# Kernel optimization log

Hardware: AMD Instinct MI355X
Metric: run time of the kernel (lower is better)

The kernel has to match this reference:

```python
import jax, jax.numpy as jnp
import numpy as np

N = 2_000_000
F = 32  # feature_num
GH = GW = 256


def _bilinear_interpolate(grid, coords):
    # grid: [H, W, F], coords: [N, 2] in (0,1)
    W = grid.shape[1] - 1
    H = grid.shape[0] - 1
    x = coords[:, 0] * W
    y = coords[:, 1] * H
    x0 = x.astype(jnp.int32)
    y0 = y.astype(jnp.int32)
    xf = x % 1
    yf = y % 1
    x1 = jnp.minimum(x0 + 1, W)
    y1 = jnp.minimum(y0 + 1, H)
    tl = grid[y0, x0]  # [N, F]
    tr = grid[y0, x1]
    bl = grid[y1, x0]
    br = grid[y1, x1]
    top = (1 - xf)[:, None] * tl + xf[:, None] * tr
    bot = (1 - xf)[:, None] * bl + xf[:, None] * br
    return (1 - yf)[:, None] * top + yf[:, None] * bot


def setup_inputs() -> dict:
    key = jax.random.key(0)
    ks = jax.random.split(key, 16)
    inp = {
        "pos": jax.random.uniform(ks[0], (N, 2), dtype=jnp.float32),
        "dir": jax.random.uniform(ks[1], (N, 2), dtype=jnp.float32),
        # grids: randn * 10 as in the torch module
        "pos_grid": jax.random.normal(ks[2], (GH, GW, F), dtype=jnp.float32) * 10.0,
        "dir_grid": jax.random.normal(ks[3], (GH, GW, F), dtype=jnp.float32) * 10.0,
        # shared encoder: Linear(2,4), Linear(4,3)
        "enc_w1": jax.random.normal(ks[4], (2, 4), dtype=jnp.float32) * 0.5,
        "enc_b1": jax.random.normal(ks[5], (4,), dtype=jnp.float32) * 0.1,
        "enc_w2": jax.random.normal(ks[6], (4, 3), dtype=jnp.float32) * 0.5,
        "enc_b2": jax.random.normal(ks[7], (3,), dtype=jnp.float32) * 0.1,
        # fc head: 2F -> 64 -> 16 -> 8 -> 3
        "fc_w1": jax.random.normal(ks[8], (2 * F, 64), dtype=jnp.float32) * 0.1,
        "fc_b1": jnp.zeros((64,), dtype=jnp.float32),
        "fc_w2": jax.random.normal(ks[9], (64, 16), dtype=jnp.float32) * 0.1,
        "fc_b2": jnp.zeros((16,), dtype=jnp.float32),
        "fc_w3": jax.random.normal(ks[10], (16, 8), dtype=jnp.float32) * 0.1,
        "fc_b3": jnp.zeros((8,), dtype=jnp.float32),
        "fc_w4": jax.random.normal(ks[11], (8, 3), dtype=jnp.float32) * 0.1,
        "fc_b4": jnp.zeros((3,), dtype=jnp.float32),
    }
    return inp


def reference(pos, dir, pos_grid, dir_grid,
              enc_w1, enc_b1, enc_w2, enc_b2,
              fc_w1, fc_b1, fc_w2, fc_b2, fc_w3, fc_b3, fc_w4, fc_b4):
    def encoder(x):
        h = jnp.tanh(x @ enc_w1 + enc_b1)
        return jax.nn.sigmoid(h @ enc_w2 + enc_b2)  # [N, 3]; only cols 0,1 used

    p = encoder(pos)
    d = encoder(dir)
    # features are .detach()'ed in the original
    pos_feat = jax.lax.stop_gradient(_bilinear_interpolate(pos_grid, p))
    dir_feat = jax.lax.stop_gradient(_bilinear_interpolate(dir_grid, d))
    x = jnp.concatenate([pos_feat, dir_feat], axis=1)  # [N, 2F]
    # Dropout layers are identity in eval mode
    x = jax.nn.leaky_relu(x @ fc_w1 + fc_b1)
    x = jax.nn.leaky_relu(x @ fc_w2 + fc_b2)
    x = jax.nn.leaky_relu(x @ fc_w3 + fc_b3)
    x = jax.nn.leaky_relu(x @ fc_w4 + fc_b4)
    return jax.nn.sigmoid(x) * 255.0
```

## Files before the change

kernel.cpp:

```cpp
#include <hip/hip_runtime.h>
#include <math.h>

typedef __attribute__((ext_vector_type(8))) __bf16 bf16x8;
typedef __attribute__((ext_vector_type(4))) __bf16 bf16x4;
typedef __attribute__((ext_vector_type(4))) short short4v;
typedef __attribute__((ext_vector_type(4))) float floatx4;
typedef __attribute__((ext_vector_type(8))) float floatx8;

__device__ __forceinline__ float fast_rcp(float x) { return __builtin_amdgcn_rcpf(x); }
__device__ __forceinline__ float sigmoidf_(float z) { return fast_rcp(1.0f + __expf(-z)); }
__device__ __forceinline__ float fast_tanh(float z) {
    float e = __expf(2.0f * z);
    return 1.0f - 2.0f * fast_rcp(e + 1.0f);
}
__device__ __forceinline__ float leaky(float v) { return fmaxf(v, 0.01f * v); }

__device__ __forceinline__ int swzb(int row, int byteoff) {
    return row * 128 + (byteoff ^ ((row & 7) << 4));
}

__global__ void convert_grids(const float* __restrict__ g0, const float* __restrict__ g1,
                              __bf16* __restrict__ o0, __bf16* __restrict__ o1, int elems) {
    int i = blockIdx.x * blockDim.x + threadIdx.x;
    int nvec = elems >> 2;
    if (i < nvec) {
        float4 v = ((const float4*)g0)[i];
        bf16x4 r = { (__bf16)v.x, (__bf16)v.y, (__bf16)v.z, (__bf16)v.w };
        ((bf16x4*)o0)[i] = r;
    } else if (i < 2 * nvec) {
        int j = i - nvec;
        float4 v = ((const float4*)g1)[j];
        bf16x4 r = { (__bf16)v.x, (__bf16)v.y, (__bf16)v.z, (__bf16)v.w };
        ((bf16x4*)o1)[j] = r;
    }
}

template<bool BF16G>
__global__ __launch_bounds__(256, 3) void gridnet_fwd(
    const float2* __restrict__ pos, const float2* __restrict__ dir_,
    const float* __restrict__ pos_gridf, const float* __restrict__ dir_gridf,
    const __bf16* __restrict__ pos_gridb, const __bf16* __restrict__ dir_gridb,
    const float* __restrict__ enc_w1, const float* __restrict__ enc_b1,
    const float* __restrict__ enc_w2, const float* __restrict__ enc_b2,
    const float* __restrict__ fc_w1, const float* __restrict__ fc_b1,
    const float* __restrict__ fc_w2, const float* __restrict__ fc_b2,
    const float* __restrict__ fc_w3, const float* __restrict__ fc_b3,
    const float* __restrict__ fc_w4, const float* __restrict__ fc_b4,
    float* __restrict__ out, int n)
{
    __shared__ __align__(1024) char smem[8192 + 2048 + 4 * 5120];
    __shared__ float b1lds[64];
    __shared__ float b2lds[16];

    const int tid  = threadIdx.x;
    const int lane = tid & 63;
    const int wid  = tid >> 6;
    const int quad = lane >> 4;
    const int l15  = lane & 15;

    char* W1p = smem;
    char* W2p = smem + 8192;
    float* H2f = (float*)(smem + 10240 + wid * 5120);

    for (int idx = tid; idx < 4096; idx += 256)
        *(__bf16*)(W1p + swzb(idx & 63, (idx >> 6) * 2)) = (__bf16)fc_w1[idx];
    for (int idx = tid; idx < 1024; idx += 256)
        *(__bf16*)(W2p + swzb(idx & 15, (idx >> 4) * 2)) = (__bf16)fc_w2[idx];
    if (tid < 64) b1lds[tid] = fc_b1[tid];
    if (tid < 16) b2lds[tid] = fc_b2[tid];
    __syncthreads();

    bf16x8 wf[2][4];
    #pragma unroll
    for (int ks = 0; ks < 2; ++ks)
        #pragma unroll
        for (int mt = 0; mt < 4; ++mt)
            wf[ks][mt] = *(const bf16x8*)(W1p + swzb(mt * 16 + l15, ks * 64 + quad * 16));
    short4v w2a[4];
    #pragma unroll
    for (int kb = 0; kb < 4; ++kb)
        w2a[kb] = *(const short4v*)(W2p + swzb(l15, kb * 32 + quad * 8));
    floatx4 b1v[4];
    #pragma unroll
    for (int mt = 0; mt < 4; ++mt)
        b1v[mt] = *(const floatx4*)(b1lds + mt * 16 + quad * 4);
    floatx4 b2v = *(const floatx4*)(b2lds + quad * 4);

    int i  = blockIdx.x * 256 + wid * 64 + lane;
    int ic = min(i, n - 1);

    unsigned pcp[2];
    float xfp[2], yfp[2];
    #pragma unroll
    for (int pass = 0; pass < 2; ++pass) {
        float2 xy = pass ? dir_[ic] : pos[ic];
        float hh[4];
        #pragma unroll
        for (int k = 0; k < 4; ++k)
            hh[k] = fast_tanh(xy.x * enc_w1[k] + xy.y * enc_w1[4 + k] + enc_b1[k]);
        float e0 = enc_b2[0], e1 = enc_b2[1];
        #pragma unroll
        for (int k = 0; k < 4; ++k) {
            e0 += hh[k] * enc_w2[3 * k + 0];
            e1 += hh[k] * enc_w2[3 * k + 1];
        }
        float x = sigmoidf_(e0) * 255.0f;
        float y = sigmoidf_(e1) * 255.0f;
        int x0 = (int)x, y0 = (int)y;
        xfp[pass] = x - (float)x0;
        yfp[pass] = y - (float)y0;
        int x1 = min(x0 + 1, 255), y1 = min(y0 + 1, 255);
        pcp[pass] = (unsigned)x0 | ((unsigned)y0 << 8) | ((unsigned)x1 << 16) | ((unsigned)y1 << 24);
    }

    bf16x8 xfr[2][4];
    #pragma unroll
    for (int ks = 0; ks < 2; ++ks) {
        #pragma unroll
        for (int nt = 0; nt < 4; ++nt) {
            const int src = nt * 16 + l15;
            unsigned pcq = (unsigned)__shfl((int)pcp[ks], src);
            float xfq = __shfl(xfp[ks], src);
            float yfq = __shfl(yfp[ks], src);
            int x0 = pcq & 255, y0 = (pcq >> 8) & 255;
            int x1 = (pcq >> 16) & 255, y1 = pcq >> 24;
            float oxf = 1.0f - xfq, oyf = 1.0f - yfq;
            floatx8 r;
            if (BF16G) {
                const __bf16* ga = (ks ? dir_gridb : pos_gridb) + quad * 8;
                bf16x8 va = *(const bf16x8*)(ga + (((y0 << 8) + x0) << 5));
                bf16x8 vb = *(const bf16x8*)(ga + (((y0 << 8) + x1) << 5));
                bf16x8 vc = *(const bf16x8*)(ga + (((y1 << 8) + x0) << 5));
                bf16x8 vd = *(const bf16x8*)(ga + (((y1 << 8) + x1) << 5));
                r = (oyf * oxf) * __builtin_convertvector(va, floatx8)
                  + (oyf * xfq) * __builtin_convertvector(vb, floatx8)
                  + (yfq * oxf) * __builtin_convertvector(vc, floatx8)
                  + (yfq * xfq) * __builtin_convertvector(vd, floatx8);
            } else {
                const float* ga = (ks ? dir_gridf : pos_gridf) + quad * 8;
                floatx8 va = *(const floatx8*)(ga + (((y0 << 8) + x0) << 5));
                floatx8 vb = *(const floatx8*)(ga + (((y0 << 8) + x1) << 5));
                floatx8 vc = *(const floatx8*)(ga + (((y1 << 8) + x0) << 5));
                floatx8 vd = *(const floatx8*)(ga + (((y1 << 8) + x1) << 5));
                r = (oyf * oxf) * va + (oyf * xfq) * vb + (yfq * oxf) * vc + (yfq * xfq) * vd;
            }
            xfr[ks][nt] = __builtin_convertvector(r, bf16x8);
        }
    }

    floatx4 acc[4][4];
    #pragma unroll
    for (int mt = 0; mt < 4; ++mt)
        #pragma unroll
        for (int nt = 0; nt < 4; ++nt)
            acc[mt][nt] = b1v[mt];
    #pragma unroll
    for (int ks = 0; ks < 2; ++ks)
        #pragma unroll
        for (int mt = 0; mt < 4; ++mt)
            #pragma unroll
            for (int nt = 0; nt < 4; ++nt)
                acc[mt][nt] = __builtin_amdgcn_mfma_f32_16x16x32_bf16(wf[ks][mt], xfr[ks][nt], acc[mt][nt], 0, 0, 0);

    floatx4 acc2[4];
    #pragma unroll
    for (int nt = 0; nt < 4; ++nt) acc2[nt] = b2v;
    #pragma unroll
    for (int kb = 0; kb < 4; ++kb) {
        #pragma unroll
        for (int nt = 0; nt < 4; ++nt) {
            bf16x4 hv;
            #pragma unroll
            for (int r = 0; r < 4; ++r)
                hv[r] = (__bf16)leaky(acc[kb][nt][r]);
            acc2[nt] = __builtin_amdgcn_mfma_f32_16x16x16bf16_1k(
                w2a[kb], __builtin_bit_cast(short4v, hv), acc2[nt], 0, 0, 0);
        }
    }

    #pragma unroll
    for (int nt = 0; nt < 4; ++nt) {
        floatx4 hv;
        #pragma unroll
        for (int r = 0; r < 4; ++r)
            hv[r] = leaky(acc2[nt][r]);
        *(floatx4*)(H2f + (nt * 16 + l15) * 20 + quad * 4) = hv;
    }
    __asm__ volatile("s_waitcnt lgkmcnt(0)" ::: "memory");

    float h2[16];
    #pragma unroll
    for (int c = 0; c < 4; ++c) {
        floatx4 v = *(const floatx4*)(H2f + lane * 20 + c * 4);
        h2[4 * c + 0] = v[0]; h2[4 * c + 1] = v[1]; h2[4 * c + 2] = v[2]; h2[4 * c + 3] = v[3];
    }
    float h3[8];
    #pragma unroll
    for (int j = 0; j < 8; ++j) h3[j] = fc_b3[j];
    #pragma unroll
    for (int k = 0; k < 16; ++k) {
        float xv = h2[k];
        #pragma unroll
        for (int j = 0; j < 8; ++j) h3[j] = fmaf(xv, fc_w3[(k << 3) + j], h3[j]);
    }
    #pragma unroll
    for (int j = 0; j < 8; ++j) h3[j] = leaky(h3[j]);

    float o[3];
    #pragma unroll
    for (int j = 0; j < 3; ++j) o[j] = fc_b4[j];
    #pragma unroll
    for (int k = 0; k < 8; ++k) {
        float xv = h3[k];
        #pragma unroll
        for (int j = 0; j < 3; ++j) o[j] = fmaf(xv, fc_w4[3 * k + j], o[j]);
    }
    if (i < n) {
        #pragma unroll
        for (int j = 0; j < 3; ++j)
            out[3 * i + j] = sigmoidf_(leaky(o[j])) * 255.0f;
    }
}

extern "C" void kernel_launch(void* const* d_in, const int* in_sizes, int n_in,
                              void* d_out, int out_size, void* d_ws, size_t ws_size,
                              hipStream_t stream) {
    int n = in_sizes[0] / 2;
    const int GELEMS = 256 * 256 * 32;
    bool use_bf16 = ws_size >= (size_t)(2 * GELEMS * sizeof(__bf16));
    __bf16* g0 = (__bf16*)d_ws;
    __bf16* g1 = g0 + GELEMS;

    if (use_bf16) {
        int total = 2 * (GELEMS / 4);
        convert_grids<<<(total + 255) / 256, 256, 0, stream>>>(
            (const float*)d_in[2], (const float*)d_in[3], g0, g1, GELEMS);
    }

    int blocks = (n + 255) / 256;
    if (use_bf16) {
        gridnet_fwd<true><<<blocks, 256, 0, stream>>>(
            (const float2*)d_in[0], (const float2*)d_in[1],
            (const float*)d_in[2], (const float*)d_in[3], g0, g1,
            (const float*)d_in[4], (const float*)d_in[5],
            (const float*)d_in[6], (const float*)d_in[7],
            (const float*)d_in[8], (const float*)d_in[9],
            (const float*)d_in[10], (const float*)d_in[11],
            (const float*)d_in[12], (const float*)d_in[13],
            (const float*)d_in[14], (const float*)d_in[15],
            (float*)d_out, n);
    } else {
        gridnet_fwd<false><<<blocks, 256, 0, stream>>>(
            (const float2*)d_in[0], (const float2*)d_in[1],
            (const float*)d_in[2], (const float*)d_in[3], g0, g1,
            (const float*)d_in[4], (const float*)d_in[5],
            (const float*)d_in[6], (const float*)d_in[7],
            (const float*)d_in[8], (const float*)d_in[9],
            (const float*)d_in[10], (const float*)d_in[11],
            (const float*)d_in[12], (const float*)d_in[13],
            (const float*)d_in[14], (const float*)d_in[15],
            (float*)d_out, n);
    }
}
```

Baseline: 218.8 us.

## Run fc layers 3 and 4 as bf16 MFMAs instead of scalar FMAs

Replaces the per-lane scalar evaluation of the 16->8 and 8->3 layers with two small 16x16x16 bf16 MFMA steps. The weights are stored transposed and zero-padded in LDS, and the fc_w4 rows are replicated so each lane can pick its own point's outputs from the accumulator tiles. This removes the per-wave LDS transpose of H2 along with its wait, and about 150 scalar FMAs per point. It also shrinks shared memory by roughly 20 KB, which may allow more resident blocks. The cost is extra bf16 rounding on these layers' activations and weights.

```diff
diff --git a/kernel.cpp b/kernel.cpp
--- a/kernel.cpp
+++ b/kernel.cpp
@@ -48,9 +48,11 @@
     const float* __restrict__ fc_w4, const float* __restrict__ fc_b4,
     float* __restrict__ out, int n)
 {
-    __shared__ __align__(1024) char smem[8192 + 2048 + 4 * 5120];
+    __shared__ __align__(1024) char smem[8192 + 2048 + 512 + 512];
     __shared__ float b1lds[64];
     __shared__ float b2lds[16];
+    __shared__ float b3lds[16];
+    __shared__ float b4lds[4];
 
     const int tid  = threadIdx.x;
     const int lane = tid & 63;
@@ -60,14 +62,22 @@
 
     char* W1p = smem;
     char* W2p = smem + 8192;
-    float* H2f = (float*)(smem + 10240 + wid * 5120);
+    __bf16* W3t = (__bf16*)(smem + 10240);
+    __bf16* W4t = (__bf16*)(smem + 10752);
 
     for (int idx = tid; idx < 4096; idx += 256)
         *(__bf16*)(W1p + swzb(idx & 63, (idx >> 6) * 2)) = (__bf16)fc_w1[idx];
     for (int idx = tid; idx < 1024; idx += 256)
         *(__bf16*)(W2p + swzb(idx & 15, (idx >> 4) * 2)) = (__bf16)fc_w2[idx];
+    {
+        int m = tid >> 4, k = tid & 15;
+        W3t[tid] = (m < 8) ? (__bf16)fc_w3[k * 8 + m] : (__bf16)0.0f;
+        W4t[tid] = (k < 8 && (m & 3) < 3) ? (__bf16)fc_w4[k * 3 + (m & 3)] : (__bf16)0.0f;
+    }
     if (tid < 64) b1lds[tid] = fc_b1[tid];
     if (tid < 16) b2lds[tid] = fc_b2[tid];
+    if (tid < 16) b3lds[tid] = (tid < 8) ? fc_b3[tid] : 0.0f;
+    if (tid < 4)  b4lds[tid] = (tid < 3) ? fc_b4[tid] : 0.0f;
     __syncthreads();
 
     bf16x8 wf[2][4];
@@ -178,47 +188,41 @@
         }
     }
 
+    short4v w3a = *(const short4v*)(W3t + l15 * 16 + quad * 4);
+    short4v w4a = *(const short4v*)(W4t + l15 * 16 + quad * 4);
+    floatx4 b3v = *(const floatx4*)(b3lds + quad * 4);
+    floatx4 b4v = *(const floatx4*)(b4lds);
+
+    floatx4 acc3[4];
     #pragma unroll
     for (int nt = 0; nt < 4; ++nt) {
-        floatx4 hv;
+        bf16x4 hv;
         #pragma unroll
         for (int r = 0; r < 4; ++r)
-            hv[r] = leaky(acc2[nt][r]);
-        *(floatx4*)(H2f + (nt * 16 + l15) * 20 + quad * 4) = hv;
-    }
-    __asm__ volatile("s_waitcnt lgkmcnt(0)" ::: "memory");
-
-    float h2[16];
-    #pragma unroll
-    for (int c = 0; c < 4; ++c) {
-        floatx4 v = *(const floatx4*)(H2f + lane * 20 + c * 4);
-        h2[4 * c + 0] = v[0]; h2[4 * c + 1] = v[1]; h2[4 * c + 2] = v[2]; h2[4 * c + 3] = v[3];
-    }
-    float h3[8];
-    #pragma unroll
-    for (int j = 0; j < 8; ++j) h3[j] = fc_b3[j];
-    #pragma unroll
-    for (int k = 0; k < 16; ++k) {
-        float xv = h2[k];
-        #pragma unroll
-        for (int j = 0; j < 8; ++j) h3[j] = fmaf(xv, fc_w3[(k << 3) + j], h3[j]);
-    }
-    #pragma unroll
-    for (int j = 0; j < 8; ++j) h3[j] = leaky(h3[j]);
-
-    float o[3];
-    #pragma unroll
-    for (int j = 0; j < 3; ++j) o[j] = fc_b4[j];
-    #pragma unroll
-    for (int k = 0; k < 8; ++k) {
-        float xv = h3[k];
-        #pragma unroll
-        for (int j = 0; j < 3; ++j) o[j] = fmaf(xv, fc_w4[3 * k + j], o[j]);
-    }
+            hv[r] = (__bf16)leaky(acc2[nt][r]);
+        acc3[nt] = __builtin_amdgcn_mfma_f32_16x16x16bf16_1k(
+            w3a, __builtin_bit_cast(short4v, hv), b3v, 0, 0, 0);
+    }
+
+    floatx4 acc4[4];
+    #pragma unroll
+    for (int nt = 0; nt < 4; ++nt) {
+        bf16x4 hv;
+        #pragma unroll
+        for (int r = 0; r < 4; ++r)
+            hv[r] = (__bf16)leaky(acc3[nt][r]);
+        acc4[nt] = __builtin_amdgcn_mfma_f32_16x16x16bf16_1k(
+            w4a, __builtin_bit_cast(short4v, hv), b4v, 0, 0, 0);
+    }
+
     if (i < n) {
         #pragma unroll
-        for (int j = 0; j < 3; ++j)
-            out[3 * i + j] = sigmoidf_(leaky(o[j])) * 255.0f;
+        for (int r = 0; r < 3; ++r) {
+            float a = (quad & 1) ? acc4[1][r] : acc4[0][r];
+            float b = (quad & 1) ? acc4[3][r] : acc4[2][r];
+            float ov = (quad & 2) ? b : a;
+            out[3 * i + r] = sigmoidf_(leaky(ov)) * 255.0f;
+        }
     }
 }
 
```

New measurement: 227.9 us. +4.1%, slower.

## Duplicate right-neighbour texels into bf16 grid layout for paired gathers

Applied to the files above, without the earlier changes.

The grid conversion kernel now writes each cell's own features followed by its right neighbour's features (x+1, clamped), doubling the bf16 grid size. The gather then reads the two horizontal corners from one contiguous 128-byte span per row, which should improve cache-line locality and cut address arithmetic. The weight and bias fragment loads from LDS move to after the gather, which shortens their register lifetime. The cost is a conversion pass and workspace footprint twice as large, and the bf16 path is only taken if the workspace is big enough for it.

```diff
diff --git a/kernel.cpp b/kernel.cpp
--- a/kernel.cpp
+++ b/kernel.cpp
@@ -19,20 +19,21 @@
     return row * 128 + (byteoff ^ ((row & 7) << 4));
 }
 
-__global__ void convert_grids(const float* __restrict__ g0, const float* __restrict__ g1,
-                              __bf16* __restrict__ o0, __bf16* __restrict__ o1, int elems) {
-    int i = blockIdx.x * blockDim.x + threadIdx.x;
-    int nvec = elems >> 2;
-    if (i < nvec) {
-        float4 v = ((const float4*)g0)[i];
-        bf16x4 r = { (__bf16)v.x, (__bf16)v.y, (__bf16)v.z, (__bf16)v.w };
-        ((bf16x4*)o0)[i] = r;
-    } else if (i < 2 * nvec) {
-        int j = i - nvec;
-        float4 v = ((const float4*)g1)[j];
-        bf16x4 r = { (__bf16)v.x, (__bf16)v.y, (__bf16)v.z, (__bf16)v.w };
-        ((bf16x4*)o1)[j] = r;
-    }
+#define DUPELEMS (256 * 256 * 64)
+
+__global__ void convert_grids_dup(const float* __restrict__ g0, const float* __restrict__ g1,
+                                  __bf16* __restrict__ o0, __bf16* __restrict__ o1) {
+    int j = blockIdx.x * blockDim.x + threadIdx.x;
+    int grid = j >> 19;
+    int r = j & ((1 << 19) - 1);
+    int cell = r >> 3;
+    int chunk = r & 7;
+    int y = cell >> 8, x = cell & 255;
+    int xs = (chunk & 4) ? min(x + 1, 255) : x;
+    const float* src = (grid ? g1 : g0) + (((y << 8) + xs) << 5) + (chunk & 3) * 8;
+    __bf16* dst = (grid ? o1 : o0) + cell * 64 + chunk * 8;
+    floatx8 v = *(const floatx8*)src;
+    *(bf16x8*)dst = __builtin_convertvector(v, bf16x8);
 }
 
 template<bool BF16G>
@@ -70,22 +71,6 @@
     if (tid < 16) b2lds[tid] = fc_b2[tid];
     __syncthreads();
 
-    bf16x8 wf[2][4];
-    #pragma unroll
-    for (int ks = 0; ks < 2; ++ks)
-        #pragma unroll
-        for (int mt = 0; mt < 4; ++mt)
-            wf[ks][mt] = *(const bf16x8*)(W1p + swzb(mt * 16 + l15, ks * 64 + quad * 16));
-    short4v w2a[4];
-    #pragma unroll
-    for (int kb = 0; kb < 4; ++kb)
-        w2a[kb] = *(const short4v*)(W2p + swzb(l15, kb * 32 + quad * 8));
-    floatx4 b1v[4];
-    #pragma unroll
-    for (int mt = 0; mt < 4; ++mt)
-        b1v[mt] = *(const floatx4*)(b1lds + mt * 16 + quad * 4);
-    floatx4 b2v = *(const floatx4*)(b2lds + quad * 4);
-
     int i  = blockIdx.x * 256 + wid * 64 + lane;
     int ic = min(i, n - 1);
 
@@ -109,8 +94,8 @@
         int x0 = (int)x, y0 = (int)y;
         xfp[pass] = x - (float)x0;
         yfp[pass] = y - (float)y0;
-        int x1 = min(x0 + 1, 255), y1 = min(y0 + 1, 255);
-        pcp[pass] = (unsigned)x0 | ((unsigned)y0 << 8) | ((unsigned)x1 << 16) | ((unsigned)y1 << 24);
+        int y1 = min(y0 + 1, 255);
+        pcp[pass] = (unsigned)x0 | ((unsigned)y0 << 8) | ((unsigned)y1 << 16);
     }
 
     bf16x8 xfr[2][4];
@@ -122,21 +107,23 @@
             unsigned pcq = (unsigned)__shfl((int)pcp[ks], src);
             float xfq = __shfl(xfp[ks], src);
             float yfq = __shfl(yfp[ks], src);
-            int x0 = pcq & 255, y0 = (pcq >> 8) & 255;
-            int x1 = (pcq >> 16) & 255, y1 = pcq >> 24;
+            int x0 = pcq & 255, y0 = (pcq >> 8) & 255, y1 = (pcq >> 16) & 255;
             float oxf = 1.0f - xfq, oyf = 1.0f - yfq;
             floatx8 r;
             if (BF16G) {
                 const __bf16* ga = (ks ? dir_gridb : pos_gridb) + quad * 8;
-                bf16x8 va = *(const bf16x8*)(ga + (((y0 << 8) + x0) << 5));
-                bf16x8 vb = *(const bf16x8*)(ga + (((y0 << 8) + x1) << 5));
-                bf16x8 vc = *(const bf16x8*)(ga + (((y1 << 8) + x0) << 5));
-                bf16x8 vd = *(const bf16x8*)(ga + (((y1 << 8) + x1) << 5));
+                const __bf16* p0 = ga + (((y0 << 8) + x0) << 6);
+                const __bf16* p1 = ga + (((y1 << 8) + x0) << 6);
+                bf16x8 va = *(const bf16x8*)(p0);
+                bf16x8 vb = *(const bf16x8*)(p0 + 32);
+                bf16x8 vc = *(const bf16x8*)(p1);
+                bf16x8 vd = *(const bf16x8*)(p1 + 32);
                 r = (oyf * oxf) * __builtin_convertvector(va, floatx8)
                   + (oyf * xfq) * __builtin_convertvector(vb, floatx8)
                   + (yfq * oxf) * __builtin_convertvector(vc, floatx8)
                   + (yfq * xfq) * __builtin_convertvector(vd, floatx8);
             } else {
+                int x1 = min(x0 + 1, 255);
                 const float* ga = (ks ? dir_gridf : pos_gridf) + quad * 8;
                 floatx8 va = *(const floatx8*)(ga + (((y0 << 8) + x0) << 5));
                 floatx8 vb = *(const floatx8*)(ga + (((y0 << 8) + x1) << 5));
@@ -148,6 +135,22 @@
         }
     }
 
+    bf16x8 wf[2][4];
+    #pragma unroll
+    for (int ks = 0; ks < 2; ++ks)
+        #pragma unroll
+        for (int mt = 0; mt < 4; ++mt)
+            wf[ks][mt] = *(const bf16x8*)(W1p + swzb(mt * 16 + l15, ks * 64 + quad * 16));
+    short4v w2a[4];
+    #pragma unroll
+    for (int kb = 0; kb < 4; ++kb)
+        w2a[kb] = *(const short4v*)(W2p + swzb(l15, kb * 32 + quad * 8));
+    floatx4 b1v[4];
+    #pragma unroll
+    for (int mt = 0; mt < 4; ++mt)
+        b1v[mt] = *(const floatx4*)(b1lds + mt * 16 + quad * 4);
+    floatx4 b2v = *(const floatx4*)(b2lds + quad * 4);
+
     floatx4 acc[4][4];
     #pragma unroll
     for (int mt = 0; mt < 4; ++mt)
@@ -226,15 +229,14 @@
                               void* d_out, int out_size, void* d_ws, size_t ws_size,
                               hipStream_t stream) {
     int n = in_sizes[0] / 2;
-    const int GELEMS = 256 * 256 * 32;
-    bool use_bf16 = ws_size >= (size_t)(2 * GELEMS * sizeof(__bf16));
+    bool use_bf16 = ws_size >= (size_t)(2 * DUPELEMS * sizeof(__bf16));
     __bf16* g0 = (__bf16*)d_ws;
-    __bf16* g1 = g0 + GELEMS;
+    __bf16* g1 = g0 + DUPELEMS;
 
     if (use_bf16) {
-        int total = 2 * (GELEMS / 4);
-        convert_grids<<<(total + 255) / 256, 256, 0, stream>>>(
-            (const float*)d_in[2], (const float*)d_in[3], g0, g1, GELEMS);
+        int total = 2 * (DUPELEMS / 8);
+        convert_grids_dup<<<(total + 255) / 256, 256, 0, stream>>>(
+            (const float*)d_in[2], (const float*)d_in[3], g0, g1);
     }
 
     int blocks = (n + 255) / 256;
```

Result: slower. 247.1 us (+12.9%).
